# Performance work log

Measured on AMD Instinct MI355X. Metric: run time of the kernel, lower is better.

The kernel has to match this reference:

```python
import jax, jax.numpy as jnp
import numpy as np

H, D, G = 8, 64, 64          # num_heads, head_dim, num_slices
HID = H * D                  # 512
EPS = 1e-5
N = 100000


def setup_inputs() -> dict:
    key = jax.random.key(0)
    ks = jax.random.split(key, 16)
    s = 0.02  # init scale
    return {
        "x": jax.random.normal(ks[0], (N, HID), dtype=jnp.float32),
        # x_proj / fx_proj: Linear(HID -> HID) with bias, eqx stores W as (out, in)
        "Wx": jax.random.normal(ks[1], (HID, HID), dtype=jnp.float32) * s,
        "bx": jax.random.normal(ks[2], (HID,), dtype=jnp.float32) * s,
        "Wfx": jax.random.normal(ks[3], (HID, HID), dtype=jnp.float32) * s,
        "bfx": jax.random.normal(ks[4], (HID,), dtype=jnp.float32) * s,
        # slice_proj: Linear(D -> G) with bias
        "Ws": jax.random.normal(ks[5], (G, D), dtype=jnp.float32) * s,
        "bs": jax.random.normal(ks[6], (G,), dtype=jnp.float32) * s,
        # learned temperature, init 0.5, shape (H,1,1)
        "temperature": jnp.ones((H, 1, 1), dtype=jnp.float32) * 0.5,
        # slice MultiheadAttention (num_heads=1, size D): q/k/v/out proj, no biases (eqx defaults)
        "Wq": jax.random.normal(ks[7], (D, D), dtype=jnp.float32) * s,
        "Wk": jax.random.normal(ks[8], (D, D), dtype=jnp.float32) * s,
        "Wv": jax.random.normal(ks[9], (D, D), dtype=jnp.float32) * s,
        "Wo": jax.random.normal(ks[10], (D, D), dtype=jnp.float32) * s,
        # out_proj: Linear(HID -> HID) with bias
        "Wout": jax.random.normal(ks[11], (HID, HID), dtype=jnp.float32) * s,
        "bout": jax.random.normal(ks[12], (HID,), dtype=jnp.float32) * s,
    }


def reference(x, Wx, bx, Wfx, bfx, Ws, bs, temperature, Wq, Wk, Wv, Wo, Wout, bout):
    n = x.shape[0]
    # token projections, split into heads: (H, N, D)
    x_mid = (x @ Wx.T + bx).reshape(n, H, D).transpose(1, 0, 2)
    fx_mid = (x @ Wfx.T + bfx).reshape(n, H, D).transpose(1, 0, 2)

    # slice weights: proj -> temperature-scaled softmax over G  (H, N, G)
    logits = jnp.einsum('hnd,gd->hng', x_mid, Ws) + bs
    w = jax.nn.softmax(logits * temperature, axis=-1)

    # weighted pooling to slice tokens (H, G, D)
    norm = w.sum(axis=1)                                   # (H, G)
    tokens = jnp.einsum('hnd,hng->hgd', fx_mid, w) / (norm[..., None] + EPS)

    # small single-head attention over the G slice tokens, vmapped over H
    q = jnp.einsum('hgd,od->hgo', tokens, Wq)
    k = jnp.einsum('hgd,od->hgo', tokens, Wk)
    v = jnp.einsum('hgd,od->hgo', tokens, Wv)
    attn = jax.nn.softmax(jnp.einsum('hgd,hkd->hgk', q, k) / jnp.sqrt(jnp.float32(D)), axis=-1)
    out_tok = jnp.einsum('hgk,hkd->hgd', attn, v)
    out_tok = jnp.einsum('hgd,od->hgo', out_tok, Wo)

    # deslice: weighted unpooling back to tokens, merge heads, output projection
    out = jnp.einsum('hgd,hng->hnd', out_tok, w)           # (H, N, D)
    out = out.transpose(1, 0, 2).reshape(n, HID)
    return out @ Wout.T + bout
```

## Files before the change

kernel.cpp:

```cpp
#include <hip/hip_runtime.h>
#include <hip/hip_bf16.h>

#define HID 512
#define NH  8
#define DD  64
#define GG  64
#define EPSF 1e-5f

typedef __attribute__((ext_vector_type(8))) short short8;
typedef __attribute__((ext_vector_type(4))) short short4v;
typedef __attribute__((ext_vector_type(4))) float floatx4;

__device__ __forceinline__ short f2bf(float f) {
    union { float f; unsigned u; } v; v.f = f;
    unsigned r = v.u + 0x7fffu + ((v.u >> 16) & 1u);
    return (short)(r >> 16);
}
__device__ __forceinline__ float bf2f(short s) {
    union { unsigned u; float f; } v;
    v.u = ((unsigned)(unsigned short)s) << 16;
    return v.f;
}

#define GLOAD_LDS16(g, l) __builtin_amdgcn_global_load_lds( \
    (const __attribute__((address_space(1))) unsigned int*)(g), \
    (__attribute__((address_space(3))) unsigned int*)(l), 16, 0, 0)

__global__ __launch_bounds__(256)
void cast_kernel(const float* __restrict__ x, short* __restrict__ xb, int n8) {
    int i = blockIdx.x * 256 + threadIdx.x;
    if (i >= n8) return;
    const float4* p = (const float4*)(x + (size_t)i * 8);
    float4 a = p[0], b = p[1];
    short8 v;
    v[0] = f2bf(a.x); v[1] = f2bf(a.y); v[2] = f2bf(a.z); v[3] = f2bf(a.w);
    v[4] = f2bf(b.x); v[5] = f2bf(b.y); v[6] = f2bf(b.z); v[7] = f2bf(b.w);
    *(short8*)(xb + (size_t)i * 8) = v;
}

__global__ void fold1_kernel(const float* __restrict__ Wx, const float* __restrict__ bx,
                             const float* __restrict__ Wfx, const float* __restrict__ bfx,
                             const float* __restrict__ Ws, const float* __restrict__ bs,
                             const float* __restrict__ temp,
                             short* __restrict__ Wcat, float* __restrict__ bias_cat) {
    int idx = blockIdx.x * 256 + threadIdx.x;
    int row = idx >> 9;
    int k = idx & 511;
    float val;
    if (row < 512) {
        val = Wfx[row * 512 + k];
        if (k == 0) bias_cat[row] = bfx[row];
    } else {
        int hg = row - 512;
        int h = hg >> 6, g = hg & 63;
        float t = temp[h];
        float s = 0.f;
        #pragma unroll 8
        for (int d = 0; d < 64; ++d) s += Ws[g * 64 + d] * Wx[(h * 64 + d) * 512 + k];
        val = s * t;
        if (k == 0) {
            float b = 0.f;
            for (int d = 0; d < 64; ++d) b += Ws[g * 64 + d] * bx[h * 64 + d];
            bias_cat[row] = (b + bs[g]) * t;
        }
    }
    Wcat[idx] = f2bf(val);
}

template <bool OUT_F32, bool FUSE_SM>
__global__ __launch_bounds__(256, 4)
void gemm_bt(const short* __restrict__ A, int lda,
             const short* __restrict__ B,
             const float* __restrict__ bias,
             void* __restrict__ Cp, int ldc,
             int M, int K, int clog2, int Rtiles) {
    __shared__ short As[128 * 32];
    __shared__ short Bs[128 * 32];

    const int id = blockIdx.x;
    const int xcd = id & 7;
    const int s = id >> 3;
    const int cblk = s & ((1 << clog2) - 1);
    const int slice = (Rtiles + 7) >> 3;
    const int rt = xcd * slice + (s >> clog2);
    if (rt >= Rtiles) return;

    const int tid = threadIdx.x;
    const int wid = tid >> 6, lane = tid & 63;
    const int col0 = cblk * 128;
    const int row0 = rt * 128;
    const int wm = (wid >> 1) * 64, wn = (wid & 1) * 64;
    const int lr = lane & 15, lq = lane >> 4;

    int st_row[2], st_kc[2];
    #pragma unroll
    for (int it = 0; it < 2; ++it) {
        int c = tid + it * 256;
        st_row[it] = c >> 2;
        st_kc[it] = (c & 3) ^ ((st_row[it] >> 1) & 3);
    }
    const int fx_ = lq ^ ((lr >> 1) & 3);

    floatx4 acc[4][4];
    #pragma unroll
    for (int i = 0; i < 4; ++i)
        #pragma unroll
        for (int j = 0; j < 4; ++j) acc[i][j] = (floatx4)(0.f);

    const short* Abase = A + (size_t)row0 * lda;
    const short* Bbase = B + (size_t)col0 * lda;

    for (int k0 = 0; k0 < K; k0 += 32) {
        #pragma unroll
        for (int it = 0; it < 2; ++it) {
            short* ldsA = As + (wid * 64 + it * 256) * 8;
            short* ldsB = Bs + (wid * 64 + it * 256) * 8;
            GLOAD_LDS16(Abase + (size_t)st_row[it] * lda + k0 + st_kc[it] * 8, ldsA);
            GLOAD_LDS16(Bbase + (size_t)st_row[it] * lda + k0 + st_kc[it] * 8, ldsB);
        }
        __syncthreads();

        short8 af[4], bfr[4];
        #pragma unroll
        for (int i = 0; i < 4; ++i) af[i]  = *(const short8*)&As[(wm + i * 16 + lr) * 32 + fx_ * 8];
        #pragma unroll
        for (int j = 0; j < 4; ++j) bfr[j] = *(const short8*)&Bs[(wn + j * 16 + lr) * 32 + fx_ * 8];
        #pragma unroll
        for (int i = 0; i < 4; ++i)
            #pragma unroll
            for (int j = 0; j < 4; ++j)
                acc[i][j] = __builtin_amdgcn_mfma_f32_16x16x32_bf16(af[i], bfr[j], acc[i][j], 0, 0, 0);
        __syncthreads();
    }

    const bool do_sm = FUSE_SM && (col0 >= 512);
    float bcol[4];
    #pragma unroll
    for (int j = 0; j < 4; ++j) bcol[j] = bias[col0 + wn + j * 16 + lr];

    #pragma unroll
    for (int i = 0; i < 4; ++i) {
        #pragma unroll
        for (int r = 0; r < 4; ++r) {
            int grow = row0 + wm + i * 16 + lq * 4 + r;
            float v[4];
            #pragma unroll
            for (int j = 0; j < 4; ++j) v[j] = acc[i][j][r] + bcol[j];
            if (do_sm) {
                float m = fmaxf(fmaxf(v[0], v[1]), fmaxf(v[2], v[3]));
                #pragma unroll
                for (int off = 1; off < 16; off <<= 1) m = fmaxf(m, __shfl_xor(m, off));
                float sum = 0.f;
                #pragma unroll
                for (int j = 0; j < 4; ++j) { v[j] = __expf(v[j] - m); sum += v[j]; }
                #pragma unroll
                for (int off = 1; off < 16; off <<= 1) sum += __shfl_xor(sum, off);
                float inv = 1.f / sum;
                #pragma unroll
                for (int j = 0; j < 4; ++j) v[j] *= inv;
            }
            if (grow < M) {
                #pragma unroll
                for (int j = 0; j < 4; ++j) {
                    int gcol = col0 + wn + j * 16 + lr;
                    if constexpr (OUT_F32) ((float*)Cp)[(size_t)grow * ldc + gcol] = v[j];
                    else                   ((short*)Cp)[(size_t)grow * ldc + gcol] = f2bf(v[j]);
                }
            }
        }
    }
}

__global__ __launch_bounds__(256)
void pool_mfma(const short* __restrict__ mid, float* __restrict__ tok_raw,
               float* __restrict__ norm, int N, int chunk) {
    const int h = blockIdx.y;
    const int n0 = blockIdx.x * chunk;
    if (n0 >= N) return;
    const int ksteps = (min(chunk, N - n0)) >> 5;

    const int tid = threadIdx.x;
    const int wid = tid >> 6, lane = tid & 63;
    const int lr = lane & 15, lq = lane >> 4;
    const int wg = (wid >> 1) * 32, wd = (wid & 1) * 32;

    __shared__ short wt[32 * 72];
    __shared__ short ft[32 * 72];

    const int sn = tid >> 3;
    const int sc0 = (tid & 7) * 8;
    const int scr = (sc0 + 16 * ((sn >> 3) & 3)) & 63;
    const int st_off = sn * 72 + scr;

    const int ra = ((wg + lr) + 16 * lq) & 63;
    const int rb = ((wd + lr) + 16 * lq) & 63;

    const short* wbase = mid + (size_t)n0 * 1024 + 512 + h * 64;
    const short* fbase = mid + (size_t)n0 * 1024 + h * 64;

    floatx4 acc[2][2];
    #pragma unroll
    for (int i = 0; i < 2; ++i)
        #pragma unroll
        for (int j = 0; j < 2; ++j) acc[i][j] = (floatx4)(0.f);
    floatx4 accn[2];
    accn[0] = (floatx4)(0.f); accn[1] = (floatx4)(0.f);

    short8 ones;
    #pragma unroll
    for (int j = 0; j < 8; ++j) ones[j] = (short)0x3F80;

    for (int ks = 0; ks < ksteps; ++ks) {
        const size_t roff = (size_t)(ks * 32 + sn) * 1024;
        short8 wv = *(const short8*)(wbase + roff + sc0);
        short8 fv = *(const short8*)(fbase + roff + sc0);
        __syncthreads();
        *(short8*)&wt[st_off] = wv;
        *(short8*)&ft[st_off] = fv;
        __syncthreads();

        short8 af[2], bf_[2];
        #pragma unroll
        for (int i = 0; i < 2; ++i) {
            short tmpv[8];
            #pragma unroll
            for (int j = 0; j < 8; ++j)
                tmpv[j] = wt[(lq * 8 + j) * 72 + ((ra + i * 16) & 63)];
            af[i] = *(const short8*)tmpv;
        }
        #pragma unroll
        for (int j2 = 0; j2 < 2; ++j2) {
            short tmpv[8];
            #pragma unroll
            for (int j = 0; j < 8; ++j)
                tmpv[j] = ft[(lq * 8 + j) * 72 + ((rb + j2 * 16) & 63)];
            bf_[j2] = *(const short8*)tmpv;
        }
        #pragma unroll
        for (int i = 0; i < 2; ++i)
            #pragma unroll
            for (int j = 0; j < 2; ++j)
                acc[i][j] = __builtin_amdgcn_mfma_f32_16x16x32_bf16(af[i], bf_[j], acc[i][j], 0, 0, 0);
        if (wd == 0) {
            #pragma unroll
            for (int i = 0; i < 2; ++i)
                accn[i] = __builtin_amdgcn_mfma_f32_16x16x32_bf16(af[i], ones, accn[i], 0, 0, 0);
        }
    }

    #pragma unroll
    for (int i = 0; i < 2; ++i) {
        #pragma unroll
        for (int r = 0; r < 4; ++r) {
            int g = wg + i * 16 + lq * 4 + r;
            #pragma unroll
            for (int j = 0; j < 2; ++j) {
                int d = wd + j * 16 + lr;
                atomicAdd(&tok_raw[(h * 64 + g) * 64 + d], acc[i][j][r]);
            }
        }
    }
    if (wd == 0 && lr == 0) {
        #pragma unroll
        for (int i = 0; i < 2; ++i)
            #pragma unroll
            for (int r = 0; r < 4; ++r)
                atomicAdd(&norm[h * 64 + wg + i * 16 + lq * 4 + r], accn[i][r]);
    }
}

__global__ __launch_bounds__(256)
void attn_kernel(const float* __restrict__ tok_raw, const float* __restrict__ norm,
                 const float* __restrict__ Wq, const float* __restrict__ Wk,
                 const float* __restrict__ Wv, const float* __restrict__ Wo,
                 float* __restrict__ out_tok) {
    const int h = blockIdx.x;
    const int tid = threadIdx.x;
    const int g = tid & 63, part = tid >> 6;
    const int o0 = part * 16;

    __shared__ float tk[64][65];
    __shared__ float qq[64][65];
    __shared__ float kk[64][65];
    __shared__ float vv[64][65];
    __shared__ float pp[64][65];
    __shared__ float od[64][65];

    const float inv = 1.f / (norm[h * 64 + g] + EPSF);
    #pragma unroll
    for (int dd = 0; dd < 16; ++dd) {
        int d = o0 + dd;
        tk[g][d] = tok_raw[(size_t)(h * 64 + g) * 64 + d] * inv;
    }
    __syncthreads();

    float t[64];
    #pragma unroll
    for (int d = 0; d < 64; ++d) t[d] = tk[g][d];
    #pragma unroll
    for (int oo = 0; oo < 16; ++oo) {
        int o = o0 + oo;
        float sq = 0.f, sk = 0.f, sv = 0.f;
        #pragma unroll
        for (int d = 0; d < 64; ++d) {
            float td = t[d];
            sq += td * Wq[o * 64 + d];
            sk += td * Wk[o * 64 + d];
            sv += td * Wv[o * 64 + d];
        }
        qq[g][o] = sq; kk[g][o] = sk; vv[g][o] = sv;
    }
    __syncthreads();

    float q[64];
    #pragma unroll
    for (int o = 0; o < 64; ++o) q[o] = qq[g][o];
    #pragma unroll
    for (int jj = 0; jj < 16; ++jj) {
        int j = o0 + jj;
        float s = 0.f;
        #pragma unroll
        for (int o = 0; o < 64; ++o) s += q[o] * kk[j][o];
        pp[g][j] = s * 0.125f;
    }
    __syncthreads();

    float sr[64];
    float mx = -1e30f;
    #pragma unroll
    for (int j = 0; j < 64; ++j) { sr[j] = pp[g][j]; mx = fmaxf(mx, sr[j]); }
    float sum = 0.f;
    #pragma unroll
    for (int j = 0; j < 64; ++j) { sr[j] = __expf(sr[j] - mx); sum += sr[j]; }
    const float isum = 1.f / sum;

    #pragma unroll
    for (int dd = 0; dd < 16; ++dd) {
        int d = o0 + dd;
        float a = 0.f;
        #pragma unroll
        for (int j = 0; j < 64; ++j) a += sr[j] * vv[j][d];
        od[g][d] = a * isum;
    }
    __syncthreads();

    float ot[64];
    #pragma unroll
    for (int d = 0; d < 64; ++d) ot[d] = od[g][d];
    #pragma unroll
    for (int oo = 0; oo < 16; ++oo) {
        int o = o0 + oo;
        float a = 0.f;
        #pragma unroll
        for (int d = 0; d < 64; ++d) a += ot[d] * Wo[o * 64 + d];
        out_tok[(size_t)(h * 64 + g) * 64 + o] = a;
    }
}

__global__ void fold2_kernel(const float* __restrict__ out_tok,
                             const float* __restrict__ Wout, short* __restrict__ Vbf) {
    int idx = blockIdx.x * 256 + threadIdx.x;
    int o = idx >> 9, hg = idx & 511;
    int h = hg >> 6;
    const float* ot = out_tok + (size_t)hg * 64;
    const float* wo = Wout + (size_t)o * 512 + h * 64;
    float s = 0.f;
    #pragma unroll 8
    for (int d = 0; d < 64; ++d) s += ot[d] * wo[d];
    Vbf[idx] = f2bf(s);
}

extern "C" void kernel_launch(void* const* d_in, const int* in_sizes, int n_in,
                              void* d_out, int out_size, void* d_ws, size_t ws_size,
                              hipStream_t stream) {
    const float* x    = (const float*)d_in[0];
    const float* Wx   = (const float*)d_in[1];
    const float* bx   = (const float*)d_in[2];
    const float* Wfx  = (const float*)d_in[3];
    const float* bfx  = (const float*)d_in[4];
    const float* Ws   = (const float*)d_in[5];
    const float* bs   = (const float*)d_in[6];
    const float* temp = (const float*)d_in[7];
    const float* Wq   = (const float*)d_in[8];
    const float* Wk   = (const float*)d_in[9];
    const float* Wv   = (const float*)d_in[10];
    const float* Wo   = (const float*)d_in[11];
    const float* Wout = (const float*)d_in[12];
    const float* bout = (const float*)d_in[13];

    const int N = in_sizes[0] / HID;

    char* p = (char*)d_ws;
    short* mid = (short*)p;           p += (size_t)N * 1024 * 2;
    short* Wcat = (short*)p;          p += (size_t)1024 * 512 * 2;
    float* bias_cat = (float*)p;      p += 1024 * 4;
    float* tok_raw = (float*)p;       p += (size_t)NH * GG * DD * 4;
    float* norm_ = (float*)p;         p += (size_t)NH * GG * 4;
    float* out_tok = (float*)p;       p += (size_t)NH * GG * DD * 4;
    short* Vbf = (short*)p;           p += (size_t)512 * 512 * 2;
    short* x_bf = (short*)d_out;

    cast_kernel<<<(N * 512 / 8 + 255) / 256, 256, 0, stream>>>(x, x_bf, N * 512 / 8);
    fold1_kernel<<<2048, 256, 0, stream>>>(Wx, bx, Wfx, bfx, Ws, bs, temp, Wcat, bias_cat);

    const int R = (N + 127) / 128;
    const int slice = (R + 7) / 8;

    gemm_bt<false, true><<<8 * slice * 8, 256, 0, stream>>>(
        x_bf, HID, Wcat, bias_cat, (void*)mid, 1024, N, 512, 3, R);

    hipMemsetAsync(tok_raw, 0, (size_t)(NH * GG * DD + NH * GG) * 4, stream);

    const int chunk = 544;
    dim3 g2((N + chunk - 1) / chunk, 8);
    pool_mfma<<<g2, 256, 0, stream>>>(mid, tok_raw, norm_, N, chunk);

    attn_kernel<<<8, 256, 0, stream>>>(tok_raw, norm_, Wq, Wk, Wv, Wo, out_tok);

    fold2_kernel<<<1024, 256, 0, stream>>>(out_tok, Wout, Vbf);

    gemm_bt<true, false><<<8 * slice * 4, 256, 0, stream>>>(
        mid + 512, 1024, Vbf, bout, d_out, HID, N, 512, 2, R);
}
```

Baseline: 778.6 us.

## Replace 128x128 GEMM with 256x256 double-buffered pipelined 512-thread GEMM

Swaps the 128x128-tile, 256-thread GEMM, which synchronised on every K-step, for a 256x256-tile, 512-thread kernel. The new kernel double-buffers 64-wide K slices in LDS and spreads async global-to-LDS loads across the MFMA phases, gated by explicit vmcnt waits and barriers. It raises wave priority around the MFMA bursts and hardcodes K=512. The aim is more operand reuse per load and hiding load latency behind compute, at the cost of about 128KB of LDS per block, higher register pressure, and a fixed K.

New measurement: 813.8 us. 1.05x slower.

```diff
diff --git a/kernel.cpp b/kernel.cpp
--- a/kernel.cpp
+++ b/kernel.cpp
@@ -8,7 +8,6 @@
 #define EPSF 1e-5f
 
 typedef __attribute__((ext_vector_type(8))) short short8;
-typedef __attribute__((ext_vector_type(4))) short short4v;
 typedef __attribute__((ext_vector_type(4))) float floatx4;
 
 __device__ __forceinline__ short f2bf(float f) {
@@ -68,14 +67,14 @@
 }
 
 template <bool OUT_F32, bool FUSE_SM>
-__global__ __launch_bounds__(256, 4)
-void gemm_bt(const short* __restrict__ A, int lda,
+__global__ __launch_bounds__(512, 2)
+void gemm256(const short* __restrict__ A, int lda,
              const short* __restrict__ B,
              const float* __restrict__ bias,
              void* __restrict__ Cp, int ldc,
-             int M, int K, int clog2, int Rtiles) {
-    __shared__ short As[128 * 32];
-    __shared__ short Bs[128 * 32];
+             int M, int clog2, int Rtiles) {
+    __shared__ short As[2][256 * 64];
+    __shared__ short Bs[2][256 * 64];
 
     const int id = blockIdx.x;
     const int xcd = id & 7;
@@ -86,63 +85,109 @@
     if (rt >= Rtiles) return;
 
     const int tid = threadIdx.x;
-    const int wid = tid >> 6, lane = tid & 63;
-    const int col0 = cblk * 128;
-    const int row0 = rt * 128;
-    const int wm = (wid >> 1) * 64, wn = (wid & 1) * 64;
+    const int wid = tid >> 6;
+    const int lane = tid & 63;
+    const int wm = wid >> 2, wn = wid & 3;
     const int lr = lane & 15, lq = lane >> 4;
-
-    int st_row[2], st_kc[2];
-    #pragma unroll
-    for (int it = 0; it < 2; ++it) {
-        int c = tid + it * 256;
-        st_row[it] = c >> 2;
-        st_kc[it] = (c & 3) ^ ((st_row[it] >> 1) & 3);
-    }
-    const int fx_ = lq ^ ((lr >> 1) & 3);
-
-    floatx4 acc[4][4];
-    #pragma unroll
-    for (int i = 0; i < 4; ++i)
+    const int row0 = rt * 256, col0 = cblk * 256;
+
+    const int srow = tid >> 3;
+    const int schunk = (tid & 7) ^ (srow & 7);
+    const short* Asrc = A + (size_t)(row0 + srow) * lda + schunk * 8;
+    const short* Bsrc = B + (size_t)(col0 + srow) * lda + schunk * 8;
+    const int ldst = wid * 512;
+
+#define SA(buf, kt, Lk) GLOAD_LDS16(Asrc + (size_t)((Lk) * 64) * lda + (kt) * 64, \
+                                    &As[buf][(Lk) * 4096 + ldst])
+#define SB(buf, kt, Lk) GLOAD_LDS16(Bsrc + (size_t)((Lk) * 64) * lda + (kt) * 64, \
+                                    &Bs[buf][(Lk) * 4096 + ldst])
+
+    const int axor = lr & 7;
+    const int coff0 = (lq ^ axor) * 8;
+    const int coff1 = ((4 + lq) ^ axor) * 8;
+    const int aoff = (wm * 128 + lr) * 64;
+    const int boff = (wn * 64 + lr) * 64;
+
+    floatx4 acc[8][4];
+    #pragma unroll
+    for (int i = 0; i < 8; ++i)
         #pragma unroll
         for (int j = 0; j < 4; ++j) acc[i][j] = (floatx4)(0.f);
 
-    const short* Abase = A + (size_t)row0 * lda;
-    const short* Bbase = B + (size_t)col0 * lda;
-
-    for (int k0 = 0; k0 < K; k0 += 32) {
-        #pragma unroll
-        for (int it = 0; it < 2; ++it) {
-            short* ldsA = As + (wid * 64 + it * 256) * 8;
-            short* ldsB = Bs + (wid * 64 + it * 256) * 8;
-            GLOAD_LDS16(Abase + (size_t)st_row[it] * lda + k0 + st_kc[it] * 8, ldsA);
-            GLOAD_LDS16(Bbase + (size_t)st_row[it] * lda + k0 + st_kc[it] * 8, ldsB);
-        }
-        __syncthreads();
-
-        short8 af[4], bfr[4];
-        #pragma unroll
-        for (int i = 0; i < 4; ++i) af[i]  = *(const short8*)&As[(wm + i * 16 + lr) * 32 + fx_ * 8];
-        #pragma unroll
-        for (int j = 0; j < 4; ++j) bfr[j] = *(const short8*)&Bs[(wn + j * 16 + lr) * 32 + fx_ * 8];
-        #pragma unroll
-        for (int i = 0; i < 4; ++i)
-            #pragma unroll
-            for (int j = 0; j < 4; ++j)
-                acc[i][j] = __builtin_amdgcn_mfma_f32_16x16x32_bf16(af[i], bfr[j], acc[i][j], 0, 0, 0);
-        __syncthreads();
-    }
+    SA(0, 0, 0); SA(0, 0, 1); SA(0, 0, 2); SA(0, 0, 3);
+    SB(0, 0, 0); SB(0, 0, 1); SB(0, 0, 2); SB(0, 0, 3);
+    SB(1, 1, 0); SB(1, 1, 1); SB(1, 1, 2); SB(1, 1, 3);
+    SA(1, 1, 0); SA(1, 1, 2);
+    asm volatile("s_waitcnt vmcnt(6)" ::: "memory");
+    __builtin_amdgcn_s_barrier();
+
+    short8 bfr[4][2];
+    short8 af[2][2];
+
+    #pragma unroll 1
+    for (int u = 0; u < 4; ++u) {
+        const int st = (u < 3);
+        #pragma unroll
+        for (int cb = 0; cb < 2; ++cb) {
+            #pragma unroll
+            for (int p = 0; p < 4; ++p) {
+                const int q = cb * 4 + p;
+                if (p == 0) {
+                    #pragma unroll
+                    for (int j = 0; j < 4; ++j) {
+                        bfr[j][0] = *(const short8*)&Bs[cb][boff + j * 1024 + coff0];
+                        bfr[j][1] = *(const short8*)&Bs[cb][boff + j * 1024 + coff1];
+                    }
+                }
+                #pragma unroll
+                for (int i2 = 0; i2 < 2; ++i2) {
+                    af[i2][0] = *(const short8*)&As[cb][aoff + (2 * p + i2) * 1024 + coff0];
+                    af[i2][1] = *(const short8*)&As[cb][aoff + (2 * p + i2) * 1024 + coff1];
+                }
+                if (q == 0)      { SA(1, 2 * u + 1, 1); SA(1, 2 * u + 1, 3); }
+                else if (st) {
+                    if (q == 1)      { SB(0, 2 * u + 2, 0); SB(0, 2 * u + 2, 1); }
+                    else if (q == 2) { SB(0, 2 * u + 2, 2); SB(0, 2 * u + 2, 3); }
+                    else if (q == 3) { SA(0, 2 * u + 2, 0); SA(0, 2 * u + 2, 2); }
+                    else if (q == 4) { SA(0, 2 * u + 2, 1); SA(0, 2 * u + 2, 3); }
+                    else if (q == 5) { SB(1, 2 * u + 3, 0); SB(1, 2 * u + 3, 1); }
+                    else if (q == 6) { SB(1, 2 * u + 3, 2); SB(1, 2 * u + 3, 3); }
+                    else             { SA(1, 2 * u + 3, 0); SA(1, 2 * u + 3, 2); }
+                }
+                if (q == 3) {
+                    if (st) asm volatile("s_waitcnt vmcnt(6)" ::: "memory");
+                    else    asm volatile("s_waitcnt vmcnt(0)" ::: "memory");
+                } else if (q == 7 && st) {
+                    asm volatile("s_waitcnt vmcnt(6)" ::: "memory");
+                }
+                __builtin_amdgcn_s_barrier();
+                __builtin_amdgcn_s_setprio(1);
+                #pragma unroll
+                for (int ks = 0; ks < 2; ++ks)
+                    #pragma unroll
+                    for (int i2 = 0; i2 < 2; ++i2)
+                        #pragma unroll
+                        for (int j = 0; j < 4; ++j)
+                            acc[2 * p + i2][j] = __builtin_amdgcn_mfma_f32_16x16x32_bf16(
+                                af[i2][ks], bfr[j][ks], acc[2 * p + i2][j], 0, 0, 0);
+                __builtin_amdgcn_s_setprio(0);
+                __builtin_amdgcn_s_barrier();
+            }
+        }
+    }
+#undef SA
+#undef SB
+
+    float bcol[4];
+    #pragma unroll
+    for (int j = 0; j < 4; ++j) bcol[j] = bias[col0 + wn * 64 + j * 16 + lr];
 
     const bool do_sm = FUSE_SM && (col0 >= 512);
-    float bcol[4];
-    #pragma unroll
-    for (int j = 0; j < 4; ++j) bcol[j] = bias[col0 + wn + j * 16 + lr];
-
-    #pragma unroll
-    for (int i = 0; i < 4; ++i) {
+    #pragma unroll
+    for (int i = 0; i < 8; ++i) {
         #pragma unroll
         for (int r = 0; r < 4; ++r) {
-            int grow = row0 + wm + i * 16 + lq * 4 + r;
+            const int grow = row0 + wm * 128 + i * 16 + lq * 4 + r;
             float v[4];
             #pragma unroll
             for (int j = 0; j < 4; ++j) v[j] = acc[i][j][r] + bcol[j];
@@ -155,14 +200,14 @@
                 for (int j = 0; j < 4; ++j) { v[j] = __expf(v[j] - m); sum += v[j]; }
                 #pragma unroll
                 for (int off = 1; off < 16; off <<= 1) sum += __shfl_xor(sum, off);
-                float inv = 1.f / sum;
+                const float inv = 1.f / sum;
                 #pragma unroll
                 for (int j = 0; j < 4; ++j) v[j] *= inv;
             }
             if (grow < M) {
                 #pragma unroll
                 for (int j = 0; j < 4; ++j) {
-                    int gcol = col0 + wn + j * 16 + lr;
+                    const int gcol = col0 + wn * 64 + j * 16 + lr;
                     if constexpr (OUT_F32) ((float*)Cp)[(size_t)grow * ldc + gcol] = v[j];
                     else                   ((short*)Cp)[(size_t)grow * ldc + gcol] = f2bf(v[j]);
                 }
@@ -403,11 +448,11 @@
     cast_kernel<<<(N * 512 / 8 + 255) / 256, 256, 0, stream>>>(x, x_bf, N * 512 / 8);
     fold1_kernel<<<2048, 256, 0, stream>>>(Wx, bx, Wfx, bfx, Ws, bs, temp, Wcat, bias_cat);
 
-    const int R = (N + 127) / 128;
+    const int R = (N + 255) / 256;
     const int slice = (R + 7) / 8;
 
-    gemm_bt<false, true><<<8 * slice * 8, 256, 0, stream>>>(
-        x_bf, HID, Wcat, bias_cat, (void*)mid, 1024, N, 512, 3, R);
+    gemm256<false, true><<<8 * slice * 4, 512, 0, stream>>>(
+        x_bf, HID, Wcat, bias_cat, (void*)mid, 1024, N, 2, R);
 
     hipMemsetAsync(tok_raw, 0, (size_t)(NH * GG * DD + NH * GG) * 4, stream);
 
@@ -419,6 +464,6 @@
 
     fold2_kernel<<<1024, 256, 0, stream>>>(out_tok, Wout, Vbf);
 
-    gemm_bt<true, false><<<8 * slice * 4, 256, 0, stream>>>(
-        mid + 512, 1024, Vbf, bout, d_out, HID, N, 512, 2, R);
-}
+    gemm256<true, false><<<8 * slice * 2, 512, 0, stream>>>(
+        mid + 512, 1024, Vbf, bout, d_out, HID, N, 1, R);
+}
```
